# Kernel optimization log

Hardware: AMD Instinct MI355X
Metric: run time of the kernel (lower is better)

## Reference

```python
import jax, jax.numpy as jnp
import numpy as np

B, L, DIM, N_STATE, K_CONV = 2, 2048, 1024, 16, 4


def setup_inputs() -> dict:
    key = jax.random.key(0)
    ks = jax.random.split(key, 6)
    sc = lambda k, shape, s: jax.random.normal(k, shape, jnp.float32) * s
    return {
        "x": jax.random.normal(ks[0], (B, L, DIM), jnp.float32),
        "in_proj_w": sc(ks[1], (2 * DIM, DIM), 0.02),
        "conv_w": sc(ks[2], (DIM, 1, K_CONV), 0.1),
        "conv_b": jnp.zeros((DIM,), jnp.float32),
        "x_proj_w": sc(ks[3], (2 * N_STATE + DIM, DIM), 0.02),
        "D_param": jnp.ones((DIM,), jnp.float32),
        "out_proj_w": sc(ks[4], (DIM, DIM), 0.02),
    }


def reference(x, in_proj_w, conv_w, conv_b, x_proj_w, D_param, out_proj_w):
    b, l, d = x.shape
    n = (x_proj_w.shape[0] - d) // 2
    k = conv_w.shape[-1]
    # A buffer: -[1..n] broadcast over channels -> [d, n]
    A = -(jnp.arange(1, n + 1, dtype=x.dtype)[None, :] * jnp.ones((d, 1), x.dtype))

    xz = x @ in_proj_w.T                       # [b, l, 2d]
    x_c, z = xz[..., :d], xz[..., d:]

    # depthwise causal conv (torch pads both sides k-1 then truncates to l == left-pad k-1)
    xc = jnp.transpose(x_c, (0, 2, 1))          # [b, d, l]
    xc = jax.lax.conv_general_dilated(
        xc, conv_w, window_strides=(1,), padding=[(k - 1, 0)],
        dimension_numbers=("NCH", "OIH", "NCH"), feature_group_count=d)
    xc = xc + conv_b[None, :, None]
    xc = jax.nn.silu(jnp.transpose(xc, (0, 2, 1)))  # [b, l, d]

    x_dbl = xc @ x_proj_w.T                    # [b, l, 2n + d]
    B_ssm = x_dbl[..., :n]                     # [b, l, n]
    C_ssm = x_dbl[..., n:2 * n]                # [b, l, n]
    dt = jax.nn.softplus(x_dbl[..., 2 * n:])   # [b, l, d]

    dA = jnp.exp(dt[..., None] * A[None, None])            # [b, l, d, n]
    dBx = (dt[..., None] * B_ssm[:, :, None, :]) * xc[..., None]  # dB * x, [b, l, d, n]

    def step(h, inputs):
        dA_t, dBx_t, C_t = inputs              # [b,d,n], [b,d,n], [b,n]
        h = h * dA_t + dBx_t
        y_t = jnp.einsum("bdn,bn->bd", h, C_t)
        return h, y_t

    h0 = jnp.zeros((b, d, n), x.dtype)
    _, ys = jax.lax.scan(
        step, h0,
        (jnp.moveaxis(dA, 1, 0), jnp.moveaxis(dBx, 1, 0), jnp.moveaxis(C_ssm, 1, 0)))
    y = jnp.moveaxis(ys, 0, 1) + D_param * xc  # [b, l, d]
    y = y * jax.nn.silu(z)
    return y @ out_proj_w.T
```

## Files before the change

### kernel.cpp

```cpp
#include <hip/hip_runtime.h>
#include <cmath>

#define BB   2
#define LL   2048
#define DIMD 1024
#define NS   16
#define KC   4
#define ML   (BB*LL)
#define XZ_N (2*DIMD)
#define XD_N (2*NS + DIMD)
#define LC   16
#define NC   (LL/LC)

typedef __attribute__((ext_vector_type(8))) short bf16x8;
typedef __attribute__((ext_vector_type(4))) float f32x4;

__device__ __forceinline__ unsigned short f2bf(float f) {
    union { float f; unsigned u; } v; v.f = f;
    unsigned r = v.u + 0x7FFF + ((v.u >> 16) & 1);
    return (unsigned short)(r >> 16);
}
__device__ __forceinline__ float bf2f(unsigned short u) {
    union { unsigned u; float f; } v; v.u = (unsigned)u << 16;
    return v.f;
}
__device__ __forceinline__ float silu_f(float a) {
    return a / (1.f + __expf(-a));
}
__device__ __forceinline__ void dt_decay(float raw, float& dt, float& e) {
    const float t = __expf(fminf(raw, 80.f));
    e  = 1.f / (1.f + t);
    dt = (raw > 15.f) ? raw : -__logf(e);
}

__global__ __launch_bounds__(256) void cvt_all(
    const float* __restrict__ s0, unsigned short* __restrict__ d0, int n0,
    const float* __restrict__ s1, unsigned short* __restrict__ d1, int n1,
    const float* __restrict__ s2, unsigned short* __restrict__ d2, int n2,
    const float* __restrict__ s3, unsigned short* __restrict__ d3, int n3)
{
    int i = blockIdx.x * blockDim.x + threadIdx.x;
    const float* src; unsigned short* dst;
    if (i < n0)                { src = s0; dst = d0; }
    else if ((i -= n0) < n1)   { src = s1; dst = d1; }
    else if ((i -= n1) < n2)   { src = s2; dst = d2; }
    else if ((i -= n2) < n3)   { src = s3; dst = d3; }
    else return;
    float4 f = ((const float4*)src)[i];
    ushort4 o;
    o.x = f2bf(f.x); o.y = f2bf(f.y); o.z = f2bf(f.z); o.w = f2bf(f.w);
    ((ushort4*)dst)[i] = o;
}

template<bool CONV>
__global__ __launch_bounds__(256) void gemm_mfma_bt(
    const unsigned short* __restrict__ A,
    const unsigned short* __restrict__ Bw,
    float* __restrict__ C,
    unsigned short* __restrict__ zb,
    const float* __restrict__ cw,
    const float* __restrict__ cb,
    float* __restrict__ xcf,
    unsigned short* __restrict__ xcbo,
    int M, int N, int K, int nsplit)
{
    constexpr int AROWS = CONV ? 144 : 128;
    constexpr int XPAD  = 68;
    __shared__ short smem[2 * AROWS * 64 + 2 * 64 * 64];

    const int nwg  = gridDim.x * gridDim.y;
    int wgid = blockIdx.y * gridDim.x + blockIdx.x;
    const int cpx = nwg >> 3;
    wgid = (wgid & 7) * cpx + (wgid >> 3);
    const int bx = wgid % gridDim.x;
    const int by = wgid / gridDim.x;

    const int tid  = threadIdx.x;
    const int lane = tid & 63;
    const int wave = tid >> 6;
    const int bm = by * 128;
    const int bn = bx * 64;
    const int wm = wave * 32;
    const int l15  = lane & 15;
    const int quad = lane >> 4;

    const bool doConv = CONV && (bn < nsplit);

    f32x4 acc[2][4];
    #pragma unroll
    for (int i = 0; i < 2; ++i)
        #pragma unroll
        for (int j = 0; j < 4; ++j)
            acc[i][j] = (f32x4){0.f, 0.f, 0.f, 0.f};
    f32x4 accx = (f32x4){0.f, 0.f, 0.f, 0.f};

    const int NK = K >> 6;

    auto stage = [&](int s, int k0) {
        short* Abase = smem + (size_t)s * (AROWS * 64);
        short* Bbase = smem + 2 * (AROWS * 64) + (size_t)s * (64 * 64);
        #pragma unroll
        for (int q = 0; q < 4; ++q) {
            const int ci = q * 256 + tid;
            const int srow = ci >> 3;
            const int cc = (ci & 7) ^ (srow & 7);
            short* ldsA = Abase + (size_t)(q * 256 + (tid & ~63)) * 8;
            int ra = CONV ? (bm - 16 + srow) : (bm + srow);
            if (CONV && ra < 0) ra = 0;
            const unsigned short* ga = A + (size_t)ra * K + k0 + cc * 8;
            __builtin_amdgcn_global_load_lds(
                (const __attribute__((address_space(1))) void*)ga,
                (__attribute__((address_space(3))) void*)ldsA, 16, 0, 0);
        }
        if constexpr (CONV) {
            if (lane < 32) {
                const int ci5 = 1024 + wave * 32 + lane;
                const int srow = ci5 >> 3;
                const int cc = (ci5 & 7) ^ (srow & 7);
                short* ldsA = Abase + (size_t)(1024 + wave * 32) * 8;
                const unsigned short* ga =
                    A + (size_t)(bm - 16 + srow) * K + k0 + cc * 8;
                __builtin_amdgcn_global_load_lds(
                    (const __attribute__((address_space(1))) void*)ga,
                    (__attribute__((address_space(3))) void*)ldsA, 16, 0, 0);
            }
        }
        #pragma unroll
        for (int q = 0; q < 2; ++q) {
            const int ci = q * 256 + tid;
            const int r  = ci >> 3;
            const int cc = (ci & 7) ^ (r & 7);
            short* ldsB = Bbase + (size_t)(q * 256 + (tid & ~63)) * 8;
            int rb = bn + r; if (rb > N - 1) rb = N - 1;
            const unsigned short* gb = Bw + (size_t)rb * K + k0 + cc * 8;
            __builtin_amdgcn_global_load_lds(
                (const __attribute__((address_space(1))) void*)gb,
                (__attribute__((address_space(3))) void*)ldsB, 16, 0, 0);
        }
    };

    stage(0, 0);

    int cur = 0;
    for (int t = 0; t < NK; ++t) {
        if (t + 1 < NK) {
            stage(cur ^ 1, (t + 1) * 64);
            if constexpr (CONV)
                asm volatile("s_waitcnt vmcnt(7)" ::: "memory");
            else
                asm volatile("s_waitcnt vmcnt(6)" ::: "memory");
        } else {
            asm volatile("s_waitcnt vmcnt(0)" ::: "memory");
        }
        __builtin_amdgcn_s_barrier();

        const short* Ab = smem + (size_t)cur * (AROWS * 64);
        const short* Bb = smem + 2 * (AROWS * 64) + (size_t)cur * (64 * 64);
        #pragma unroll
        for (int kh = 0; kh < 2; ++kh) {
            bf16x8 af[2], bfr[4];
            #pragma unroll
            for (int i = 0; i < 2; ++i) {
                const int srow = (CONV ? 16 : 0) + wm + i * 16 + l15;
                const int pc  = (kh * 4 + quad) ^ (srow & 7);
                af[i] = *(const bf16x8*)(Ab + srow * 64 + pc * 8);
            }
            #pragma unroll
            for (int j = 0; j < 4; ++j) {
                const int row = j * 16 + l15;
                const int pc  = (kh * 4 + quad) ^ (row & 7);
                bfr[j] = *(const bf16x8*)(Bb + row * 64 + pc * 8);
            }
            #pragma unroll
            for (int i = 0; i < 2; ++i)
                #pragma unroll
                for (int j = 0; j < 4; ++j)
                    acc[i][j] = __builtin_amdgcn_mfma_f32_16x16x32_bf16(
                        af[i], bfr[j], acc[i][j], 0, 0, 0);
            if (doConv) {
                const int pcA = (kh * 4 + quad) ^ (l15 & 7);
                bf16x8 afx = *(const bf16x8*)(Ab + l15 * 64 + pcA * 8);
                const int rowB = wave * 16 + l15;
                const int pcB = (kh * 4 + quad) ^ (rowB & 7);
                bf16x8 bfx = *(const bf16x8*)(Bb + rowB * 64 + pcB * 8);
                accx = __builtin_amdgcn_mfma_f32_16x16x32_bf16(
                    afx, bfx, accx, 0, 0, 0);
            }
        }

        if (t + 1 < NK) __builtin_amdgcn_s_barrier();
        cur ^= 1;
    }

    if (doConv) {
        __syncthreads();
        float* xcs = (float*)smem;
        #pragma unroll
        for (int i = 0; i < 2; ++i)
            #pragma unroll
            for (int j = 0; j < 4; ++j)
                #pragma unroll
                for (int r = 0; r < 4; ++r)
                    xcs[(16 + wm + i * 16 + quad * 4 + r) * XPAD
                        + j * 16 + l15] = acc[i][j][r];
        #pragma unroll
        for (int r = 0; r < 4; ++r)
            xcs[(quad * 4 + r) * XPAD + wave * 16 + l15] = accx[r];
        __syncthreads();

        const int col = tid & 63;
        const int gc  = bn + col;
        const float4 wv  = ((const float4*)cw)[gc];
        const float  bvv = cb[gc];
        const int r0 = wave * 32;
        float xm3 = xcs[(r0 + 13) * XPAD + col];
        float xm2 = xcs[(r0 + 14) * XPAD + col];
        float xm1 = xcs[(r0 + 15) * XPAD + col];
        #pragma unroll
        for (int k = 0; k < 32; ++k) {
            const int r  = r0 + k;
            const int gr = bm + r;
            const int l  = gr & (LL - 1);
            const float xm0 = xcs[(r + 16) * XPAD + col];
            const float a = bvv + wv.x * ((l >= 3) ? xm3 : 0.f)
                                + wv.y * ((l >= 2) ? xm2 : 0.f)
                                + wv.z * ((l >= 1) ? xm1 : 0.f)
                                + wv.w * xm0;
            const float v = silu_f(a);
            xcf[(size_t)gr * DIMD + gc]  = v;
            xcbo[(size_t)gr * DIMD + gc] = f2bf(v);
            xm3 = xm2; xm2 = xm1; xm1 = xm0;
        }
    } else {
        #pragma unroll
        for (int i = 0; i < 2; ++i) {
            const int rbase = bm + wm + i * 16 + quad * 4;
            #pragma unroll
            for (int j = 0; j < 4; ++j) {
                const int colc = bn + j * 16 + l15;
                if (colc < nsplit) {
                    #pragma unroll
                    for (int r = 0; r < 4; ++r)
                        C[(size_t)(rbase + r) * nsplit + colc] = acc[i][j][r];
                } else if (colc < N) {
                    const int zc = colc - nsplit;
                    #pragma unroll
                    for (int r = 0; r < 4; ++r)
                        zb[(size_t)(rbase + r) * DIMD + zc]
                            = f2bf(silu_f(acc[i][j][r]));
                }
            }
        }
    }
}

__global__ __launch_bounds__(256) void scan_part1(const float* __restrict__ xdbl,
                                                  const float* __restrict__ xc,
                                                  float* __restrict__ hfin,
                                                  float* __restrict__ Ssum)
{
    __shared__ float Bsh[LC][NS];

    const int tid = threadIdx.x;
    const int idx = blockIdx.x * 256 + tid;
    const int d   = idx & (DIMD - 1);
    const int bc  = idx >> 10;
    const int c   = bc & (NC - 1);
    const int b   = bc >> 7;
    const int l0  = c * LC;

    const float* xdbl_p = xdbl + ((size_t)b * LL + l0) * XD_N;
    const float* xc_p   = xc   + ((size_t)b * LL + l0) * DIMD + d;

    if (tid < LC * NS / 4) {
        const int l = tid >> 2, q = tid & 3;
        ((float4*)&Bsh[l][0])[q] = ((const float4*)(xdbl_p + (size_t)l * XD_N))[q];
    }
    __syncthreads();

    float raw[LC], xcv[LC];
    #pragma unroll
    for (int i = 0; i < LC; ++i) raw[i] = xdbl_p[(size_t)i * XD_N + 2 * NS + d];
    #pragma unroll
    for (int i = 0; i < LC; ++i) xcv[i] = xc_p[(size_t)i * DIMD];

    float e[LC], dx[LC];
    float S = 0.f;
    #pragma unroll
    for (int i = 0; i < LC; ++i) {
        float dt, ev;
        dt_decay(raw[i], dt, ev);
        S += dt;
        e[i]  = ev;
        dx[i] = dt * xcv[i];
    }

    float h[NS];
    #pragma unroll
    for (int n = 0; n < NS; ++n) h[n] = 0.f;

    #pragma unroll
    for (int i = 0; i < LC; ++i) {
        const float4* BC = (const float4*)&Bsh[i][0];
        const float4 B0 = BC[0], B1 = BC[1], B2 = BC[2], B3 = BC[3];
        const float ev = e[i], dxv = dx[i];
        const float e2 = ev * ev, e4 = e2 * e2;
        float p0 = ev, p1 = e2, p2 = e2 * ev, p3 = e4;
        h[0]  = fmaf(h[0],  p0, dxv * B0.x);
        h[1]  = fmaf(h[1],  p1, dxv * B0.y);
        h[2]  = fmaf(h[2],  p2, dxv * B0.z);
        h[3]  = fmaf(h[3],  p3, dxv * B0.w);
        p0 *= e4; p1 *= e4; p2 *= e4; p3 *= e4;
        h[4]  = fmaf(h[4],  p0, dxv * B1.x);
        h[5]  = fmaf(h[5],  p1, dxv * B1.y);
        h[6]  = fmaf(h[6],  p2, dxv * B1.z);
        h[7]  = fmaf(h[7],  p3, dxv * B1.w);
        p0 *= e4; p1 *= e4; p2 *= e4; p3 *= e4;
        h[8]  = fmaf(h[8],  p0, dxv * B2.x);
        h[9]  = fmaf(h[9],  p1, dxv * B2.y);
        h[10] = fmaf(h[10], p2, dxv * B2.z);
        h[11] = fmaf(h[11], p3, dxv * B2.w);
        p0 *= e4; p1 *= e4; p2 *= e4; p3 *= e4;
        h[12] = fmaf(h[12], p0, dxv * B3.x);
        h[13] = fmaf(h[13], p1, dxv * B3.y);
        h[14] = fmaf(h[14], p2, dxv * B3.z);
        h[15] = fmaf(h[15], p3, dxv * B3.w);
    }

    float4* hf = (float4*)(hfin + (size_t)idx * NS);
    #pragma unroll
    for (int n = 0; n < 4; ++n) hf[n] = ((float4*)h)[n];
    Ssum[idx] = S;
}

#define NGRP 8
#define CPG  (NC / NGRP)
__global__ __launch_bounds__(256) void scan_combine(float* __restrict__ hfin,
                                                    const float* __restrict__ Ssum)
{
    __shared__ float Ash[2][NGRP][NS];
    __shared__ float Bsh2[2][NGRP][NS];

    const int tid = threadIdx.x;
    const int n   = tid & (NS - 1);
    const int g   = (tid >> 4) & (NGRP - 1);
    const int d2  = tid >> 7;
    const int bd  = blockIdx.x * 2 + d2;
    const int d   = bd & (DIMD - 1);
    const int b   = bd >> 10;
    const float np1 = (float)(n + 1);
    const int c0 = g * CPG;

    float e[CPG], hb[CPG];
    #pragma unroll
    for (int j = 0; j < CPG; ++j) {
        const size_t base = ((size_t)(b * NC + c0 + j) * DIMD + d);
        const float S = Ssum[base];
        hb[j] = hfin[base * NS + n];
        e[j]  = __expf(-S * np1);
    }

    float A = 1.f, Bv = 0.f;
    #pragma unroll
    for (int j = 0; j < CPG; ++j) { Bv = fmaf(Bv, e[j], hb[j]); A *= e[j]; }

    Ash[d2][g][n] = A;  Bsh2[d2][g][n] = Bv;
    __syncthreads();

    float hc = 0.f;
    for (int j = 0; j < g; ++j) hc = fmaf(hc, Ash[d2][j][n], Bsh2[d2][j][n]);

    #pragma unroll
    for (int j = 0; j < CPG; ++j) {
        const size_t o = ((size_t)(b * NC + c0 + j) * DIMD + d) * NS + n;
        hfin[o] = hc;
        hc = fmaf(hc, e[j], hb[j]);
    }
}

__global__ __launch_bounds__(256) void scan_part2(const float* __restrict__ xdbl,
                                                  const float* __restrict__ xc,
                                                  const unsigned short* __restrict__ zb,
                                                  const float* __restrict__ hfin,
                                                  const float* __restrict__ Dp,
                                                  unsigned short* __restrict__ yout)
{
    __shared__ float BCs[LC][2 * NS];

    const int tid = threadIdx.x;
    const int idx = blockIdx.x * 256 + tid;
    const int d   = idx & (DIMD - 1);
    const int bc  = idx >> 10;
    const int c   = bc & (NC - 1);
    const int b   = bc >> 7;
    const int l0  = c * LC;

    const float* xdbl_p = xdbl + ((size_t)b * LL + l0) * XD_N;
    const float* xc_p   = xc   + ((size_t)b * LL + l0) * DIMD + d;
    const unsigned short* zb_p = zb + ((size_t)b * LL + l0) * DIMD + d;
    unsigned short* y_p = yout + ((size_t)b * LL + l0) * DIMD + d;

    if (tid < LC * 2 * NS / 4) {
        const int l = tid >> 3, q = tid & 7;
        ((float4*)&BCs[l][0])[q] = ((const float4*)(xdbl_p + (size_t)l * XD_N))[q];
    }
    __syncthreads();

    float raw[LC], xcv[LC], zg[LC];
    #pragma unroll
    for (int i = 0; i < LC; ++i) raw[i] = xdbl_p[(size_t)i * XD_N + 2 * NS + d];
    #pragma unroll
    for (int i = 0; i < LC; ++i) xcv[i] = xc_p[(size_t)i * DIMD];
    #pragma unroll
    for (int i = 0; i < LC; ++i) zg[i] = bf2f(zb_p[(size_t)i * DIMD]);

    float e[LC], dx[LC];
    #pragma unroll
    for (int i = 0; i < LC; ++i) {
        float dt, ev;
        dt_decay(raw[i], dt, ev);
        e[i]  = ev;
        dx[i] = dt * xcv[i];
    }

    const float Dv = Dp[d];
    float h[NS];
    {
        const float4* hf = (const float4*)(hfin + (size_t)idx * NS);
        #pragma unroll
        for (int n = 0; n < 4; ++n) ((float4*)h)[n] = hf[n];
    }

    #pragma unroll
    for (int i = 0; i < LC; ++i) {
        const float4* BC = (const float4*)&BCs[i][0];
        const float4 B0 = BC[0], B1 = BC[1], B2 = BC[2], B3 = BC[3];
        const float4 C0 = BC[4], C1 = BC[5], C2 = BC[6], C3 = BC[7];
        const float ev = e[i], dxv = dx[i];
        const float e2 = ev * ev, e4 = e2 * e2;
        float p0 = ev, p1 = e2, p2 = e2 * ev, p3 = e4;
        float y0, y1, y2, y3;
        h[0]  = fmaf(h[0],  p0, dxv * B0.x); y0 = h[0]  * C0.x;
        h[1]  = fmaf(h[1],  p1, dxv * B0.y); y1 = h[1]  * C0.y;
        h[2]  = fmaf(h[2],  p2, dxv * B0.z); y2 = h[2]  * C0.z;
        h[3]  = fmaf(h[3],  p3, dxv * B0.w); y3 = h[3]  * C0.w;
        p0 *= e4; p1 *= e4; p2 *= e4; p3 *= e4;
        h[4]  = fmaf(h[4],  p0, dxv * B1.x); y0 = fmaf(h[4],  C1.x, y0);
        h[5]  = fmaf(h[5],  p1, dxv * B1.y); y1 = fmaf(h[5],  C1.y, y1);
        h[6]  = fmaf(h[6],  p2, dxv * B1.z); y2 = fmaf(h[6],  C1.z, y2);
        h[7]  = fmaf(h[7],  p3, dxv * B1.w); y3 = fmaf(h[7],  C1.w, y3);
        p0 *= e4; p1 *= e4; p2 *= e4; p3 *= e4;
        h[8]  = fmaf(h[8],  p0, dxv * B2.x); y0 = fmaf(h[8],  C2.x, y0);
        h[9]  = fmaf(h[9],  p1, dxv * B2.y); y1 = fmaf(h[9],  C2.y, y1);
        h[10] = fmaf(h[10], p2, dxv * B2.z); y2 = fmaf(h[10], C2.z, y2);
        h[11] = fmaf(h[11], p3, dxv * B2.w); y3 = fmaf(h[11], C2.w, y3);
        p0 *= e4; p1 *= e4; p2 *= e4; p3 *= e4;
        h[12] = fmaf(h[12], p0, dxv * B3.x); y0 = fmaf(h[12], C3.x, y0);
        h[13] = fmaf(h[13], p1, dxv * B3.y); y1 = fmaf(h[13], C3.y, y1);
        h[14] = fmaf(h[14], p2, dxv * B3.z); y2 = fmaf(h[14], C3.z, y2);
        h[15] = fmaf(h[15], p3, dxv * B3.w); y3 = fmaf(h[15], C3.w, y3);

        const float y  = (y0 + y1) + (y2 + y3);
        const float yv = fmaf(Dv, xcv[i], y);
        y_p[(size_t)i * DIMD] = f2bf(yv * zg[i]);
    }
}

extern "C" void kernel_launch(void* const* d_in, const int* in_sizes, int n_in,
                              void* d_out, int out_size, void* d_ws, size_t ws_size,
                              hipStream_t stream)
{
    const float* x          = (const float*)d_in[0];
    const float* in_proj_w  = (const float*)d_in[1];
    const float* conv_w     = (const float*)d_in[2];
    const float* conv_b     = (const float*)d_in[3];
    const float* x_proj_w   = (const float*)d_in[4];
    const float* D_param    = (const float*)d_in[5];
    const float* out_proj_w = (const float*)d_in[6];
    float* out = (float*)d_out;

    float* xcraw = (float*)d_ws;
    float* xc    = xcraw + (size_t)ML * DIMD;
    float* xdbl  = xc    + (size_t)ML * DIMD;
    unsigned short* zb  = (unsigned short*)(xdbl + (size_t)ML * XD_N);
    unsigned short* xb  = zb  + (size_t)ML * DIMD;
    unsigned short* xcb = xb  + (size_t)ML * DIMD;
    unsigned short* wb1 = xcb + (size_t)ML * DIMD;
    unsigned short* wb2 = wb1 + (size_t)XZ_N * DIMD;
    unsigned short* wb3 = wb2 + (size_t)XD_N * DIMD;
    float* hfin = (float*)(wb3 + (size_t)DIMD * DIMD);
    float* Ssum = hfin + (size_t)BB * NC * DIMD * NS;
    unsigned short* yb  = xb;

    const int n0 = ML * DIMD / 4, n1 = XZ_N * DIMD / 4,
              n2 = XD_N * DIMD / 4, n3 = DIMD * DIMD / 4;
    const int ncvt = n0 + n1 + n2 + n3;

    cvt_all<<<(ncvt + 255) / 256, 256, 0, stream>>>(
        x, xb, n0, in_proj_w, wb1, n1, x_proj_w, wb2, n2, out_proj_w, wb3, n3);

    gemm_mfma_bt<true><<<dim3(XZ_N / 64, ML / 128), 256, 0, stream>>>(
        xb, wb1, nullptr, zb, conv_w, conv_b, xc, xcb, ML, XZ_N, DIMD, DIMD);

    gemm_mfma_bt<false><<<dim3((XD_N + 63) / 64, ML / 128), 256, 0, stream>>>(
        xcb, wb2, xdbl, nullptr, nullptr, nullptr, nullptr, nullptr,
        ML, XD_N, DIMD, XD_N);

    scan_part1<<<(BB * NC * DIMD) / 256, 256, 0, stream>>>(xdbl, xc, hfin, Ssum);
    scan_combine<<<(BB * DIMD) / 2, 256, 0, stream>>>(hfin, Ssum);
    scan_part2<<<(BB * NC * DIMD) / 256, 256, 0, stream>>>(xdbl, xc, zb, hfin,
                                                           D_param, yb);

    gemm_mfma_bt<false><<<dim3(DIMD / 64, ML / 128), 256, 0, stream>>>(
        yb, wb3, out, nullptr, nullptr, nullptr, nullptr, nullptr,
        ML, DIMD, DIMD, DIMD);
}
```

Baseline: 188.9 us.

## Enlarge GEMM tiles to 128x128 with 2x2 wave layout

Widens the MFMA GEMM block tile from 128x64 to 128x128, with each wave computing a 64x64 sub-tile through 4x4 accumulators. B staging, the LDS sizes, wait counts, the fused conv epilogue and the launch grids are all adjusted to match. The goal is more arithmetic per byte of LDS and global traffic. The cost is more registers and LDS per block and half as many workgroups, which could lower occupancy and leave CUs idle on the smaller GEMMs.

Measured after the change: 196.6 us. 4.1% more time.

```diff
diff --git a/kernel.cpp b/kernel.cpp
--- a/kernel.cpp
+++ b/kernel.cpp
@@ -65,8 +65,9 @@
     int M, int N, int K, int nsplit)
 {
     constexpr int AROWS = CONV ? 144 : 128;
-    constexpr int XPAD  = 68;
-    __shared__ short smem[2 * AROWS * 64 + 2 * 64 * 64];
+    constexpr int XPAD  = 132;
+    constexpr int SMEM_SHORTS = CONV ? 38016 : (2 * 128 * 64 + 2 * 128 * 64);
+    __shared__ short smem[SMEM_SHORTS];
 
     const int nwg  = gridDim.x * gridDim.y;
     int wgid = blockIdx.y * gridDim.x + blockIdx.x;
@@ -79,26 +80,29 @@
     const int lane = tid & 63;
     const int wave = tid >> 6;
     const int bm = by * 128;
-    const int bn = bx * 64;
-    const int wm = wave * 32;
+    const int bn = bx * 128;
+    const int wm = (wave >> 1) * 64;
+    const int wn = (wave & 1) * 64;
     const int l15  = lane & 15;
     const int quad = lane >> 4;
 
     const bool doConv = CONV && (bn < nsplit);
 
-    f32x4 acc[2][4];
-    #pragma unroll
-    for (int i = 0; i < 2; ++i)
+    f32x4 acc[4][4];
+    #pragma unroll
+    for (int i = 0; i < 4; ++i)
         #pragma unroll
         for (int j = 0; j < 4; ++j)
             acc[i][j] = (f32x4){0.f, 0.f, 0.f, 0.f};
-    f32x4 accx = (f32x4){0.f, 0.f, 0.f, 0.f};
+    f32x4 accx[2];
+    accx[0] = (f32x4){0.f, 0.f, 0.f, 0.f};
+    accx[1] = (f32x4){0.f, 0.f, 0.f, 0.f};
 
     const int NK = K >> 6;
 
     auto stage = [&](int s, int k0) {
         short* Abase = smem + (size_t)s * (AROWS * 64);
-        short* Bbase = smem + 2 * (AROWS * 64) + (size_t)s * (64 * 64);
+        short* Bbase = smem + 2 * (AROWS * 64) + (size_t)s * (128 * 64);
         #pragma unroll
         for (int q = 0; q < 4; ++q) {
             const int ci = q * 256 + tid;
@@ -126,7 +130,7 @@
             }
         }
         #pragma unroll
-        for (int q = 0; q < 2; ++q) {
+        for (int q = 0; q < 4; ++q) {
             const int ci = q * 256 + tid;
             const int r  = ci >> 3;
             const int cc = (ci & 7) ^ (r & 7);
@@ -146,33 +150,33 @@
         if (t + 1 < NK) {
             stage(cur ^ 1, (t + 1) * 64);
             if constexpr (CONV)
-                asm volatile("s_waitcnt vmcnt(7)" ::: "memory");
+                asm volatile("s_waitcnt vmcnt(9)" ::: "memory");
             else
-                asm volatile("s_waitcnt vmcnt(6)" ::: "memory");
+                asm volatile("s_waitcnt vmcnt(8)" ::: "memory");
         } else {
             asm volatile("s_waitcnt vmcnt(0)" ::: "memory");
         }
         __builtin_amdgcn_s_barrier();
 
         const short* Ab = smem + (size_t)cur * (AROWS * 64);
-        const short* Bb = smem + 2 * (AROWS * 64) + (size_t)cur * (64 * 64);
+        const short* Bb = smem + 2 * (AROWS * 64) + (size_t)cur * (128 * 64);
         #pragma unroll
         for (int kh = 0; kh < 2; ++kh) {
-            bf16x8 af[2], bfr[4];
+            bf16x8 af[4], bfr[4];
             #pragma unroll
-            for (int i = 0; i < 2; ++i) {
+            for (int i = 0; i < 4; ++i) {
                 const int srow = (CONV ? 16 : 0) + wm + i * 16 + l15;
                 const int pc  = (kh * 4 + quad) ^ (srow & 7);
                 af[i] = *(const bf16x8*)(Ab + srow * 64 + pc * 8);
             }
             #pragma unroll
             for (int j = 0; j < 4; ++j) {
-                const int row = j * 16 + l15;
+                const int row = wn + j * 16 + l15;
                 const int pc  = (kh * 4 + quad) ^ (row & 7);
                 bfr[j] = *(const bf16x8*)(Bb + row * 64 + pc * 8);
             }
             #pragma unroll
-            for (int i = 0; i < 2; ++i)
+            for (int i = 0; i < 4; ++i)
                 #pragma unroll
                 for (int j = 0; j < 4; ++j)
                     acc[i][j] = __builtin_amdgcn_mfma_f32_16x16x32_bf16(
@@ -180,11 +184,20 @@
             if (doConv) {
                 const int pcA = (kh * 4 + quad) ^ (l15 & 7);
                 bf16x8 afx = *(const bf16x8*)(Ab + l15 * 64 + pcA * 8);
-                const int rowB = wave * 16 + l15;
-                const int pcB = (kh * 4 + quad) ^ (rowB & 7);
-                bf16x8 bfx = *(const bf16x8*)(Bb + rowB * 64 + pcB * 8);
-                accx = __builtin_amdgcn_mfma_f32_16x16x32_bf16(
-                    afx, bfx, accx, 0, 0, 0);
+                {
+                    const int rowB = wave * 32 + l15;
+                    const int pcB = (kh * 4 + quad) ^ (rowB & 7);
+                    bf16x8 bfx = *(const bf16x8*)(Bb + rowB * 64 + pcB * 8);
+                    accx[0] = __builtin_amdgcn_mfma_f32_16x16x32_bf16(
+                        afx, bfx, accx[0], 0, 0, 0);
+                }
+                {
+                    const int rowB = wave * 32 + 16 + l15;
+                    const int pcB = (kh * 4 + quad) ^ (rowB & 7);
+                    bf16x8 bfx = *(const bf16x8*)(Bb + rowB * 64 + pcB * 8);
+                    accx[1] = __builtin_amdgcn_mfma_f32_16x16x32_bf16(
+                        afx, bfx, accx[1], 0, 0, 0);
+                }
             }
         }
 
@@ -196,28 +209,31 @@
         __syncthreads();
         float* xcs = (float*)smem;
         #pragma unroll
-        for (int i = 0; i < 2; ++i)
+        for (int i = 0; i < 4; ++i)
             #pragma unroll
             for (int j = 0; j < 4; ++j)
                 #pragma unroll
                 for (int r = 0; r < 4; ++r)
                     xcs[(16 + wm + i * 16 + quad * 4 + r) * XPAD
-                        + j * 16 + l15] = acc[i][j][r];
-        #pragma unroll
-        for (int r = 0; r < 4; ++r)
-            xcs[(quad * 4 + r) * XPAD + wave * 16 + l15] = accx[r];
+                        + wn + j * 16 + l15] = acc[i][j][r];
+        #pragma unroll
+        for (int jx = 0; jx < 2; ++jx)
+            #pragma unroll
+            for (int r = 0; r < 4; ++r)
+                xcs[(quad * 4 + r) * XPAD + wave * 32 + jx * 16 + l15]
+                    = accx[jx][r];
         __syncthreads();
 
-        const int col = tid & 63;
+        const int col = tid & 127;
         const int gc  = bn + col;
         const float4 wv  = ((const float4*)cw)[gc];
         const float  bvv = cb[gc];
-        const int r0 = wave * 32;
+        const int r0 = (tid >> 7) * 64;
         float xm3 = xcs[(r0 + 13) * XPAD + col];
         float xm2 = xcs[(r0 + 14) * XPAD + col];
         float xm1 = xcs[(r0 + 15) * XPAD + col];
         #pragma unroll
-        for (int k = 0; k < 32; ++k) {
+        for (int k = 0; k < 64; ++k) {
             const int r  = r0 + k;
             const int gr = bm + r;
             const int l  = gr & (LL - 1);
@@ -233,11 +249,11 @@
         }
     } else {
         #pragma unroll
-        for (int i = 0; i < 2; ++i) {
+        for (int i = 0; i < 4; ++i) {
             const int rbase = bm + wm + i * 16 + quad * 4;
             #pragma unroll
             for (int j = 0; j < 4; ++j) {
-                const int colc = bn + j * 16 + l15;
+                const int colc = bn + wn + j * 16 + l15;
                 if (colc < nsplit) {
                     #pragma unroll
                     for (int r = 0; r < 4; ++r)
@@ -499,10 +515,10 @@
     cvt_all<<<(ncvt + 255) / 256, 256, 0, stream>>>(
         x, xb, n0, in_proj_w, wb1, n1, x_proj_w, wb2, n2, out_proj_w, wb3, n3);
 
-    gemm_mfma_bt<true><<<dim3(XZ_N / 64, ML / 128), 256, 0, stream>>>(
+    gemm_mfma_bt<true><<<dim3(XZ_N / 128, ML / 128), 256, 0, stream>>>(
         xb, wb1, nullptr, zb, conv_w, conv_b, xc, xcb, ML, XZ_N, DIMD, DIMD);
 
-    gemm_mfma_bt<false><<<dim3((XD_N + 63) / 64, ML / 128), 256, 0, stream>>>(
+    gemm_mfma_bt<false><<<dim3((XD_N + 127) / 128, ML / 128), 256, 0, stream>>>(
         xcb, wb2, xdbl, nullptr, nullptr, nullptr, nullptr, nullptr,
         ML, XD_N, DIMD, XD_N);
 
@@ -511,7 +527,7 @@
     scan_part2<<<(BB * NC * DIMD) / 256, 256, 0, stream>>>(xdbl, xc, zb, hfin,
                                                            D_param, yb);
 
-    gemm_mfma_bt<false><<<dim3(DIMD / 64, ML / 128), 256, 0, stream>>>(
+    gemm_mfma_bt<false><<<dim3(DIMD / 128, ML / 128), 256, 0, stream>>>(
         yb, wb3, out, nullptr, nullptr, nullptr, nullptr, nullptr,
         ML, DIMD, DIMD, DIMD);
 }
```
